# Kernel optimization log

Hardware: AMD Instinct MI355X
Metric: run time of the kernel (lower is better)

## Reference

```python
import jax, jax.numpy as jnp
import numpy as np

N_NODES = 100000
N_EDGES = 3200000
IN_DIM, HID, OUT_DIM = 1, 64, 1


def graph_conv(x, src, dst, ew, W_rel, b_rel, W_root):
    # PyG GraphConv (aggr='add'): out_i = W_rel @ sum_{j->i} w_ij x_j + b_rel + W_root @ x_i
    msg = x[src] * ew[:, None]                               # [E, F]
    agg = jax.ops.segment_sum(msg, dst, num_segments=N_NODES)  # [N, F]
    return agg @ W_rel + b_rel + x @ W_root


def setup_inputs() -> dict:
    key = jax.random.key(0)
    ks = jax.random.split(key, 12)
    def glorot(k, shape):
        fan_in, fan_out = shape
        lim = float(np.sqrt(6.0 / (fan_in + fan_out)))
        return jax.random.uniform(k, shape, jnp.float32, -lim, lim)
    x = jax.random.normal(ks[0], (N_NODES, IN_DIM), jnp.float32)
    edge_index = jax.random.randint(ks[1], (2, N_EDGES), 0, N_NODES, jnp.int64)
    edge_weight = jax.random.uniform(ks[2], (N_EDGES,), jnp.float32)
    return {
        "x": x, "edge_index": edge_index, "edge_weight": edge_weight,
        "W1_rel": glorot(ks[3], (IN_DIM, HID)), "b1": jnp.zeros((HID,), jnp.float32),
        "W1_root": glorot(ks[4], (IN_DIM, HID)),
        "W2_rel": glorot(ks[5], (HID, HID)), "b2": jnp.zeros((HID,), jnp.float32),
        "W2_root": glorot(ks[6], (HID, HID)),
        "W3_rel": glorot(ks[7], (HID, OUT_DIM)), "b3": jnp.zeros((OUT_DIM,), jnp.float32),
        "W3_root": glorot(ks[8], (HID, OUT_DIM)),
    }


def reference(x, edge_index, edge_weight, W1_rel, b1, W1_root, W2_rel, b2, W2_root, W3_rel, b3, W3_root):
    src, dst = edge_index[0], edge_index[1]
    h = graph_conv(x, src, dst, edge_weight, W1_rel, b1, W1_root)
    h = jax.nn.relu(h)  # dropout is identity in eval mode
    h = graph_conv(h, src, dst, edge_weight, W2_rel, b2, W2_root)
    h = jax.nn.relu(h)
    return graph_conv(h, src, dst, edge_weight, W3_rel, b3, W3_root)
```

## Files before the change

### kernel.cpp

```cpp
#include <hip/hip_runtime.h>

#define NN 100000
#define NE 3200000
#define HID 64
#define NPB 256
#define NB  ((NN + NPB - 1) / NPB)
#define NNP (NB * NPB)
#define CAP 9216
#define MNP 128
#define NMW (2 * NB)
#define CAPW 5120
#define CHUNK 4096
#define NCH ((NE + CHUNK - 1) / CHUNK)
#define AP 72
#define BPITCH 136
#define SRCM 0x1FFFF

typedef _Float16 half8 __attribute__((ext_vector_type(8)));
typedef _Float16 h2v   __attribute__((ext_vector_type(2)));
typedef float f32x4 __attribute__((ext_vector_type(4)));

__device__ __forceinline__ unsigned short f2hb(float v) {
    _Float16 h = (_Float16)v;
    unsigned short s;
    __builtin_memcpy(&s, &h, 2);
    return s;
}
__device__ __forceinline__ h2v ash2(unsigned int u) {
    h2v r;
    __builtin_memcpy(&r, &u, 4);
    return r;
}

__global__ __launch_bounds__(512) void k_init(const float* __restrict__ x,
                                              float2* __restrict__ sx,
                                              int* __restrict__ gcur) {
    const int i = blockIdx.x * 512 + threadIdx.x;
    if (i < NN) sx[i] = make_float2(0.f, x[i]);
    if (blockIdx.x == 0 && threadIdx.x < NB) gcur[threadIdx.x] = threadIdx.x * CAP;
}

__global__ __launch_bounds__(256) void k_scatter(const int* __restrict__ src,
                                                 const int* __restrict__ dst,
                                                 const float* __restrict__ ew,
                                                 int* __restrict__ gcur,
                                                 int2* __restrict__ rec,
                                                 unsigned char* __restrict__ dlb) {
    __shared__ int2 lrec[CHUNK];
    __shared__ unsigned short lb[CHUNK];
    __shared__ unsigned short sidx[CHUNK];
    __shared__ int cnt[NB];
    __shared__ int bme[NB];
    __shared__ int wt8[8];
    const int tid = threadIdx.x;
    const int lane = tid & 63, wvx = tid >> 6;
    for (int j = tid; j < NB; j += 256) cnt[j] = 0;
    __syncthreads();
    const long long b0 = (long long)blockIdx.x * CHUNK;
    const int valid = (int)min((long long)CHUNK, (long long)NE - b0);
    #pragma unroll
    for (int k = 0; k < CHUNK / 256; ++k) {
        int idx = k * 256 + tid;
        if (idx < valid) {
            long long e = b0 + idx;
            int d = dst[e];
            int b = d >> 8;
            lrec[idx] = make_int2(src[e] | ((d & 255) << 17), __float_as_int(ew[e]));
            lb[idx] = (unsigned short)b;
            atomicAdd(&cnt[b], 1);
        }
    }
    __syncthreads();
    int v0 = (tid < NB) ? cnt[tid] : 0;
    int v1 = (tid + 256 < NB) ? cnt[tid + 256] : 0;
    int i0 = v0, i1 = v1;
    #pragma unroll
    for (int off = 1; off < 64; off <<= 1) {
        int t0 = __shfl_up(i0, off, 64);
        int t1 = __shfl_up(i1, off, 64);
        if (lane >= off) { i0 += t0; i1 += t1; }
    }
    if (lane == 63) { wt8[wvx] = i0; wt8[4 + wvx] = i1; }
    __syncthreads();
    int off0 = 0, off1 = 0;
    #pragma unroll
    for (int j = 0; j < 8; ++j) {
        int wt = wt8[j];
        if (j < wvx) off0 += wt;
        if (j < 4 + wvx) off1 += wt;
    }
    const int excl0 = off0 + i0 - v0;
    const int excl1 = off1 + i1 - v1;
    if (tid < NB) {
        int bb = v0 ? atomicAdd(&gcur[tid], v0) : 0;
        bme[tid] = bb - excl0;
        cnt[tid] = excl0;
    }
    if (tid + 256 < NB) {
        int bb = v1 ? atomicAdd(&gcur[tid + 256], v1) : 0;
        bme[tid + 256] = bb - excl1;
        cnt[tid + 256] = excl1;
    }
    __syncthreads();
    #pragma unroll
    for (int k = 0; k < CHUNK / 256; ++k) {
        int idx = k * 256 + tid;
        if (idx < valid) {
            int sp = atomicAdd(&cnt[lb[idx]], 1);
            sidx[sp] = (unsigned short)idx;
        }
    }
    __syncthreads();
    #pragma unroll
    for (int k = 0; k < CHUNK / 256; ++k) {
        int sp = k * 256 + tid;
        if (sp < valid) {
            int idx = sidx[sp];
            int b = lb[idx];
            int2 rc = lrec[idx];
            int go = bme[b] + sp;
            rec[go] = rc;
            dlb[go] = (unsigned char)((rc.x >> 17) & 255);
        }
    }
}

__global__ __launch_bounds__(512) void k_s1(const int* __restrict__ gcur,
                                            const int2* __restrict__ rec,
                                            const float* __restrict__ x,
                                            float* __restrict__ sxf) {
    __shared__ float loc[NPB];
    if (threadIdx.x < NPB) loc[threadIdx.x] = 0.f;
    __syncthreads();
    const int wid = blockIdx.x;
    const int b = wid >> 1, j = wid & 1;
    const int beg = b * CAP, cnt = gcur[b] - beg;
    const int half = (cnt + 1) >> 1;
    const int s0 = beg + j * half;
    const int s1e = beg + min(cnt, j * half + half);
    for (int t = s0 + threadIdx.x; t < s1e; t += 512) {
        int2 rc = rec[t];
        atomicAdd(&loc[rc.x >> 17], __int_as_float(rc.y) * x[rc.x & SRCM]);
    }
    __syncthreads();
    const int i = b * NPB + threadIdx.x;
    if (threadIdx.x < NPB && i < NN) {
        float v = loc[threadIdx.x];
        if (v != 0.f) atomicAdd(&sxf[2 * i], v);
    }
}

__global__ __launch_bounds__(512) void k_pack(const int* __restrict__ gcur,
                                              const int2* __restrict__ rec,
                                              const unsigned char* __restrict__ dlb,
                                              const float2* __restrict__ sx,
                                              int4* __restrict__ rec2q,
                                              int* __restrict__ noff,
                                              unsigned char* __restrict__ ngrp) {
    __shared__ int4 img4[CAPW / 2];
    __shared__ int hist[128];
    __shared__ int exclp[128];
    __shared__ int cur[128];
    __shared__ int wt2[2];
    unsigned short* imgh = (unsigned short*)img4;
    const int tid = threadIdx.x;
    const int lane = tid & 63, wv = tid >> 6;
    const int wid = blockIdx.x;
    const int b = wid >> 1, h = wid & 1;
    for (int j = tid; j < CAPW / 2; j += 512) img4[j] = (int4){0, 0, 0, 0};
    if (tid < 128) hist[tid] = 0;
    __syncthreads();
    const int beg = b * CAP;
    const int cnt = gcur[b] - beg;
    {
        const uchar4* d4 = (const uchar4*)(dlb + beg);
        const int n4 = cnt >> 2;
        for (int t = tid; t < n4; t += 512) {
            uchar4 q = d4[t];
            if ((q.x >> 7) == h) atomicAdd(&hist[q.x & 127], 1);
            if ((q.y >> 7) == h) atomicAdd(&hist[q.y & 127], 1);
            if ((q.z >> 7) == h) atomicAdd(&hist[q.z & 127], 1);
            if ((q.w >> 7) == h) atomicAdd(&hist[q.w & 127], 1);
        }
        for (int t = (n4 << 2) + tid; t < cnt; t += 512) {
            int dl = dlb[beg + t];
            if ((dl >> 7) == h) atomicAdd(&hist[dl & 127], 1);
        }
    }
    __syncthreads();
    int pc = 0, incl = 0;
    if (tid < 128) { pc = (hist[tid] + 7) & ~7; incl = pc; }
    #pragma unroll
    for (int off = 1; off < 64; off <<= 1) {
        int tt = __shfl_up(incl, off, 64);
        if (lane >= off) incl += tt;
    }
    if (tid < 128 && lane == 63) wt2[wv] = incl;
    __syncthreads();
    if (tid < 128) {
        int e0 = ((tid >= 64) ? wt2[0] : 0) + incl - pc;
        exclp[tid] = e0;
        cur[tid] = e0;
        const int node = wid * MNP + tid;
        noff[node] = wid * CAPW + e0;
        ngrp[node] = (unsigned char)(pc >> 3);
    }
    __syncthreads();
#define PREC(RX, RY) {                                                  \
        const int dl_ = ((RX) >> 17) & 255;                             \
        if ((dl_ >> 7) == h) {                                          \
            const float w_ = __int_as_float(RY);                        \
            const float2 v_ = sx[(RX) & SRCM];                          \
            int gs_ = atomicAdd(&cur[dl_ & 127], 1);                    \
            int hb_ = (gs_ >> 1) * 8 + (gs_ & 1);                       \
            imgh[hb_]     = f2hb(w_ * v_.x);                            \
            imgh[hb_ + 2] = f2hb(w_ * v_.y);                            \
            imgh[hb_ + 4] = f2hb(w_);                                   \
        } }
    {
        const int4* r4 = (const int4*)(rec + beg);
        const int n2 = cnt >> 1;
        for (int t = tid; t < n2; t += 512) {
            int4 q = r4[t];
            PREC(q.x, q.y)
            PREC(q.z, q.w)
        }
        for (int t = (n2 << 1) + tid; t < cnt; t += 512) {
            int2 rc = rec[beg + t];
            PREC(rc.x, rc.y)
        }
    }
#undef PREC
    __syncthreads();
    int4* d4 = rec2q + (size_t)wid * (CAPW / 2);
    for (int j = tid; j < CAPW / 2; j += 512) d4[j] = img4[j];
}

__global__ __launch_bounds__(512) void k_mega(
        const int* __restrict__ noff, const unsigned char* __restrict__ ngrp,
        const char* __restrict__ rec2b, const float2* __restrict__ sx,
        const float* __restrict__ W1_rel, const float* __restrict__ W1_root,
        const float* __restrict__ b1,
        const float* __restrict__ W2_rel, const float* __restrict__ b2,
        const float* __restrict__ W2_root,
        const float* __restrict__ W3_rel, const float* __restrict__ W3_root,
        const float* __restrict__ b3,
        float* __restrict__ p, float* __restrict__ out) {
    __shared__ _Float16 aggh[MNP * AP];
    __shared__ _Float16 Bt[HID * BPITCH];
    __shared__ float2 sxl[MNP];
    const int tid = threadIdx.x;
    const int f = tid & 63;
    const int wv = tid >> 6;
    const int gi0 = blockIdx.x * MNP;

    for (int j = tid; j < MNP * AP / 2; j += 512) ((int*)aggh)[j] = 0;
    for (int idx = tid; idx < HID * HID; idx += 512) {
        int k = idx >> 6, n = idx & 63;
        Bt[n * BPITCH + k]       = (_Float16)W2_rel[idx];
        Bt[n * BPITCH + HID + k] = (_Float16)W2_root[idx];
    }
    if (tid < MNP) {
        int gi = gi0 + tid;
        sxl[tid] = (gi < NN) ? sx[gi] : make_float2(0.f, 0.f);
    }
    const float w1rf = W1_rel[f], w1tf = W1_root[f], b1ff = b1[f];
    const float b3v = b3[0];
    __syncthreads();

    {
        const int first = gi0 + wv * 16;
        int soff = __builtin_amdgcn_readfirstlane(noff[first]);
        const int4 gvv = *(const int4*)(ngrp + first);
        unsigned ua = __builtin_amdgcn_readfirstlane((unsigned)gvv.x);
        unsigned ub = __builtin_amdgcn_readfirstlane((unsigned)gvv.y);
        unsigned uc = __builtin_amdgcn_readfirstlane((unsigned)gvv.z);
        unsigned ud = __builtin_amdgcn_readfirstlane((unsigned)gvv.w);
        unsigned long long clo = (unsigned long long)ua | ((unsigned long long)ub << 32);
        unsigned long long chi = (unsigned long long)uc | ((unsigned long long)ud << 32);
        #define BSUM(u) (((u) & 255u) + (((u) >> 8) & 255u) + (((u) >> 16) & 255u) + ((u) >> 24))
        const int tg = (int)(BSUM(ua) + BSUM(ub) + BSUM(uc) + BSUM(ud));
        #undef BSUM

        const h2v w1r2 = {(_Float16)w1rf, (_Float16)w1rf};
        const h2v w1t2 = {(_Float16)w1tf, (_Float16)w1tf};
        const h2v b1f2 = {(_Float16)b1ff, (_Float16)b1ff};
        const h2v one2 = {(_Float16)1.f, (_Float16)1.f};
        const h2v zero2 = {(_Float16)0.f, (_Float16)0.f};

        float a0 = 0.f, a1 = 0.f, a2 = 0.f, a3 = 0.f;
        int nrow = wv * 16;
        const int rowend = nrow + 16;
        int grem = (int)(clo & 255); clo = (clo >> 8) | (chi << 56); chi >>= 8;
        while (grem == 0 && nrow + 1 < rowend) {
            ++nrow; grem = (int)(clo & 255);
            clo = (clo >> 8) | (chi << 56); chi >>= 8;
        }

        const int4* rp = (const int4*)rec2b + (soff >> 1);
        int4 A0, A1, A2, A3, B0, B1, B2, B3, C0, C1, C2, C3, D0, D1, D2, D3;
        if (tg >= 1) { A0 = rp[0]; A1 = rp[1]; A2 = rp[2];  A3 = rp[3]; }
        if (tg >= 2) { B0 = rp[4]; B1 = rp[5]; B2 = rp[6];  B3 = rp[7]; }
        if (tg >= 3) { C0 = rp[8]; C1 = rp[9]; C2 = rp[10]; C3 = rp[11]; }
        rp += 12;

#define PP(Q, AA) {                                          \
        h2v z_ = ash2((unsigned)(Q).z) * b1f2;               \
        z_ = ash2((unsigned)(Q).y) * w1t2 + z_;              \
        z_ = ash2((unsigned)(Q).x) * w1r2 + z_;              \
        z_ = __builtin_elementwise_max(z_, zero2);           \
        AA = __builtin_amdgcn_fdot2(z_, one2, AA, false); }

#define BNDRY() {                                                        \
        if (--grem == 0) {                                               \
            aggh[nrow * AP + f] = (_Float16)((a0 + a1) + (a2 + a3));     \
            a0 = a1 = a2 = a3 = 0.f;                                     \
            ++nrow; grem = (int)(clo & 255);                             \
            clo = (clo >> 8) | (chi << 56); chi >>= 8;                   \
            while (grem == 0 && nrow + 1 < rowend) {                     \
                ++nrow; grem = (int)(clo & 255);                         \
                clo = (clo >> 8) | (chi << 56); chi >>= 8;               \
            }                                                            \
        } }

        int t = 0;
        while (t + 4 <= tg) {
            D0 = rp[0]; D1 = rp[1]; D2 = rp[2]; D3 = rp[3];
            PP(A0, a0) PP(A1, a1) PP(A2, a2) PP(A3, a3) BNDRY(); ++t;
            A0 = rp[4]; A1 = rp[5]; A2 = rp[6]; A3 = rp[7];
            PP(B0, a0) PP(B1, a1) PP(B2, a2) PP(B3, a3) BNDRY(); ++t;
            B0 = rp[8]; B1 = rp[9]; B2 = rp[10]; B3 = rp[11];
            PP(C0, a0) PP(C1, a1) PP(C2, a2) PP(C3, a3) BNDRY(); ++t;
            C0 = rp[12]; C1 = rp[13]; C2 = rp[14]; C3 = rp[15];
            PP(D0, a0) PP(D1, a1) PP(D2, a2) PP(D3, a3) BNDRY(); ++t;
            rp += 16;
        }
        if (t < tg) {
            PP(A0, a0) PP(A1, a1) PP(A2, a2) PP(A3, a3) BNDRY(); ++t;
            if (t < tg) {
                PP(B0, a0) PP(B1, a1) PP(B2, a2) PP(B3, a3) BNDRY(); ++t;
                if (t < tg) {
                    PP(C0, a0) PP(C1, a1) PP(C2, a2) PP(C3, a3) BNDRY(); ++t;
                }
            }
        }
#undef PP
#undef BNDRY
    }
    __syncthreads();

    const int m16 = tid & 15;
    const int quad = (tid & 63) >> 4;
    f32x4 acc[4];
    #pragma unroll
    for (int c_ = 0; c_ < 4; ++c_) acc[c_] = (f32x4){0.f, 0.f, 0.f, 0.f};

    const float2 sm = sxl[wv * 16 + m16];

    #pragma unroll
    for (int kt = 0; kt < 4; ++kt) {
        const int kk = kt * 32;
        half8 af;
        if (kt < 2) {
            af = *(const half8*)&aggh[(wv * 16 + m16) * AP + kk + quad * 8];
        } else {
            const int fk0 = (kt - 2) * 32 + quad * 8;
            #pragma unroll
            for (int j = 0; j < 8; ++j) {
                const float wr = W1_rel[fk0 + j], wt = W1_root[fk0 + j], bb = b1[fk0 + j];
                af[j] = (_Float16)fmaxf(0.f, fmaf(sm.x, wr, fmaf(sm.y, wt, bb)));
            }
        }
        #pragma unroll
        for (int ct = 0; ct < 4; ++ct) {
            const half8 bfrag = *(const half8*)&Bt[(ct * 16 + m16) * BPITCH + kk + quad * 8];
            acc[ct] = __builtin_amdgcn_mfma_f32_16x16x32_f16(af, bfrag, acc[ct], 0, 0, 0);
        }
    }

    float b2c[4], w3rc[4], w3tc[4];
    #pragma unroll
    for (int ct = 0; ct < 4; ++ct) {
        const int col = ct * 16 + m16;
        b2c[ct] = b2[col]; w3rc[ct] = W3_rel[col]; w3tc[ct] = W3_root[col];
    }
    float pv[4] = {0.f, 0.f, 0.f, 0.f}, rv[4] = {0.f, 0.f, 0.f, 0.f};
    #pragma unroll
    for (int ct = 0; ct < 4; ++ct) {
        #pragma unroll
        for (int reg = 0; reg < 4; ++reg) {
            const float h2_ = fmaxf(0.f, acc[ct][reg] + b2c[ct]);
            pv[reg] = fmaf(h2_, w3rc[ct], pv[reg]);
            rv[reg] = fmaf(h2_, w3tc[ct], rv[reg]);
        }
    }
    #pragma unroll
    for (int reg = 0; reg < 4; ++reg) {
        #pragma unroll
        for (int msk = 1; msk < 16; msk <<= 1) {
            pv[reg] += __shfl_xor(pv[reg], msk, 64);
            rv[reg] += __shfl_xor(rv[reg], msk, 64);
        }
    }
    if (m16 == 0) {
        #pragma unroll
        for (int reg = 0; reg < 4; ++reg) {
            const int gi = gi0 + wv * 16 + quad * 4 + reg;
            if (gi < NN) { p[gi] = pv[reg]; out[gi] = rv[reg] + b3v; }
        }
    }
}

__global__ __launch_bounds__(512) void k_out(const int* __restrict__ gcur,
                                             const int2* __restrict__ rec,
                                             const float* __restrict__ pp,
                                             float* __restrict__ out) {
    __shared__ float loc[NPB];
    if (threadIdx.x < NPB) loc[threadIdx.x] = 0.f;
    __syncthreads();
    const int wid = blockIdx.x;
    const int b = wid >> 1, j = wid & 1;
    const int beg = b * CAP, cnt = gcur[b] - beg;
    const int half = (cnt + 1) >> 1;
    const int s0 = beg + j * half;
    const int s1e = beg + min(cnt, j * half + half);
    for (int t = s0 + threadIdx.x; t < s1e; t += 512) {
        int2 rc = rec[t];
        atomicAdd(&loc[rc.x >> 17], __int_as_float(rc.y) * pp[rc.x & SRCM]);
    }
    __syncthreads();
    const int i = b * NPB + threadIdx.x;
    if (threadIdx.x < NPB && i < NN) {
        float v = loc[threadIdx.x];
        if (v != 0.f) atomicAdd(&out[i], v);
    }
}

extern "C" void kernel_launch(void* const* d_in, const int* in_sizes, int n_in,
                              void* d_out, int out_size, void* d_ws, size_t ws_size,
                              hipStream_t stream) {
    const float* x       = (const float*)d_in[0];
    const int*   ei      = (const int*)  d_in[1];
    const float* ew      = (const float*)d_in[2];
    const float* W1_rel  = (const float*)d_in[3];
    const float* b1      = (const float*)d_in[4];
    const float* W1_root = (const float*)d_in[5];
    const float* W2_rel  = (const float*)d_in[6];
    const float* b2      = (const float*)d_in[7];
    const float* W2_root = (const float*)d_in[8];
    const float* W3_rel  = (const float*)d_in[9];
    const float* b3      = (const float*)d_in[10];
    const float* W3_root = (const float*)d_in[11];

    const int* src = ei;
    const int* dst = ei + NE;

    const size_t REC_SLOTS = (size_t)NB * CAP;
    int2*          rec   = (int2*)d_ws;
    float2*        sx    = (float2*)(rec + REC_SLOTS);
    float*         p     = (float*)(sx + NN);
    int*           noff  = (int*)(p + NN);
    unsigned char* ngrp  = (unsigned char*)(noff + NNP);
    int*           gcur  = (int*)(ngrp + NNP);
    unsigned char* dlb   = (unsigned char*)(gcur + NB);
    char*          tail  = (char*)(dlb + REC_SLOTS);
    size_t         off   = ((size_t)(tail - (char*)d_ws) + 15) & ~(size_t)15;
    char*          rec2  = (char*)d_ws + off;

    k_init<<<(NN + 511) / 512, 512, 0, stream>>>(x, sx, gcur);
    k_scatter<<<NCH, 256, 0, stream>>>(src, dst, ew, gcur, rec, dlb);
    k_s1<<<2 * NB, 512, 0, stream>>>(gcur, rec, x, (float*)sx);
    k_pack<<<NMW, 512, 0, stream>>>(gcur, rec, dlb, sx, (int4*)rec2, noff, ngrp);
    k_mega<<<NMW, 512, 0, stream>>>(noff, ngrp, rec2, sx,
                                    W1_rel, W1_root, b1,
                                    W2_rel, b2, W2_root,
                                    W3_rel, W3_root, b3, p, (float*)d_out);
    k_out<<<2 * NB, 512, 0, stream>>>(gcur, rec, p, (float*)d_out);
}
```

Baseline: 252.6 us.

## Split edge records into SoA planes with fp16 edge weights

Edge records move from interleaved int2 (packed index plus fp32 weight) to separate planes: a 32-bit packed src/dst-local array and a 16-bit fp16 weight array. The separate dst-local byte array is dropped because that value is now read back from the packed index. The packed fp16 stream used by the mega kernel is also split into three 16-bit planes (w*agg, w*x, w). This cuts the bytes written and read across scatter, s1, pack and out, and gives the mega kernel simpler contiguous loads. In exchange, edge weights are rounded to fp16 in the first-layer and output aggregations, which costs accuracy, and the mega kernel now issues three streams of loads instead of one.

Result: faster. 247.6 us (-2.0%).

```diff
diff --git a/kernel.cpp b/kernel.cpp
--- a/kernel.cpp
+++ b/kernel.cpp
@@ -26,6 +26,12 @@
     __builtin_memcpy(&s, &h, 2);
     return s;
 }
+__device__ __forceinline__ float h2f(unsigned int u) {
+    unsigned short s = (unsigned short)u;
+    _Float16 h;
+    __builtin_memcpy(&h, &s, 2);
+    return (float)h;
+}
 __device__ __forceinline__ h2v ash2(unsigned int u) {
     h2v r;
     __builtin_memcpy(&r, &u, 4);
@@ -44,9 +50,10 @@
                                                  const int* __restrict__ dst,
                                                  const float* __restrict__ ew,
                                                  int* __restrict__ gcur,
-                                                 int2* __restrict__ rec,
-                                                 unsigned char* __restrict__ dlb) {
-    __shared__ int2 lrec[CHUNK];
+                                                 int* __restrict__ rec_a,
+                                                 unsigned short* __restrict__ rec_w) {
+    __shared__ int la[CHUNK];
+    __shared__ unsigned short lw[CHUNK];
     __shared__ unsigned short lb[CHUNK];
     __shared__ unsigned short sidx[CHUNK];
     __shared__ int cnt[NB];
@@ -65,7 +72,8 @@
             long long e = b0 + idx;
             int d = dst[e];
             int b = d >> 8;
-            lrec[idx] = make_int2(src[e] | ((d & 255) << 17), __float_as_int(ew[e]));
+            la[idx] = src[e] | ((d & 255) << 17);
+            lw[idx] = f2hb(ew[e]);
             lb[idx] = (unsigned short)b;
             atomicAdd(&cnt[b], 1);
         }
@@ -117,16 +125,16 @@
         if (sp < valid) {
             int idx = sidx[sp];
             int b = lb[idx];
-            int2 rc = lrec[idx];
             int go = bme[b] + sp;
-            rec[go] = rc;
-            dlb[go] = (unsigned char)((rc.x >> 17) & 255);
+            rec_a[go] = la[idx];
+            rec_w[go] = lw[idx];
         }
     }
 }
 
 __global__ __launch_bounds__(512) void k_s1(const int* __restrict__ gcur,
-                                            const int2* __restrict__ rec,
+                                            const int* __restrict__ rec_a,
+                                            const unsigned short* __restrict__ rec_w,
                                             const float* __restrict__ x,
                                             float* __restrict__ sxf) {
     __shared__ float loc[NPB];
@@ -139,8 +147,9 @@
     const int s0 = beg + j * half;
     const int s1e = beg + min(cnt, j * half + half);
     for (int t = s0 + threadIdx.x; t < s1e; t += 512) {
-        int2 rc = rec[t];
-        atomicAdd(&loc[rc.x >> 17], __int_as_float(rc.y) * x[rc.x & SRCM]);
+        const int a = rec_a[t];
+        const float w = h2f(rec_w[t]);
+        atomicAdd(&loc[a >> 17], w * x[a & SRCM]);
     }
     __syncthreads();
     const int i = b * NPB + threadIdx.x;
@@ -151,39 +160,45 @@
 }
 
 __global__ __launch_bounds__(512) void k_pack(const int* __restrict__ gcur,
-                                              const int2* __restrict__ rec,
-                                              const unsigned char* __restrict__ dlb,
+                                              const int* __restrict__ rec_a,
+                                              const unsigned short* __restrict__ rec_w,
                                               const float2* __restrict__ sx,
-                                              int4* __restrict__ rec2q,
+                                              unsigned short* __restrict__ rec2s,
+                                              unsigned short* __restrict__ rec2x,
+                                              unsigned short* __restrict__ rec2f,
                                               int* __restrict__ noff,
                                               unsigned char* __restrict__ ngrp) {
-    __shared__ int4 img4[CAPW / 2];
+    __shared__ int4 imgq[3 * CAPW / 8];
     __shared__ int hist[128];
     __shared__ int exclp[128];
     __shared__ int cur[128];
     __shared__ int wt2[2];
-    unsigned short* imgh = (unsigned short*)img4;
+    unsigned short* img = (unsigned short*)imgq;
+    unsigned short* ws_img = img;
+    unsigned short* wx_img = img + CAPW;
+    unsigned short* wf_img = img + 2 * CAPW;
     const int tid = threadIdx.x;
     const int lane = tid & 63, wv = tid >> 6;
     const int wid = blockIdx.x;
     const int b = wid >> 1, h = wid & 1;
-    for (int j = tid; j < CAPW / 2; j += 512) img4[j] = (int4){0, 0, 0, 0};
+    for (int j = tid; j < 3 * CAPW / 8; j += 512) imgq[j] = (int4){0, 0, 0, 0};
     if (tid < 128) hist[tid] = 0;
     __syncthreads();
     const int beg = b * CAP;
     const int cnt = gcur[b] - beg;
     {
-        const uchar4* d4 = (const uchar4*)(dlb + beg);
+        const int4* a4 = (const int4*)(rec_a + beg);
         const int n4 = cnt >> 2;
         for (int t = tid; t < n4; t += 512) {
-            uchar4 q = d4[t];
-            if ((q.x >> 7) == h) atomicAdd(&hist[q.x & 127], 1);
-            if ((q.y >> 7) == h) atomicAdd(&hist[q.y & 127], 1);
-            if ((q.z >> 7) == h) atomicAdd(&hist[q.z & 127], 1);
-            if ((q.w >> 7) == h) atomicAdd(&hist[q.w & 127], 1);
+            int4 q = a4[t];
+            int d0 = q.x >> 17, d1 = q.y >> 17, d2 = q.z >> 17, d3 = q.w >> 17;
+            if ((d0 >> 7) == h) atomicAdd(&hist[d0 & 127], 1);
+            if ((d1 >> 7) == h) atomicAdd(&hist[d1 & 127], 1);
+            if ((d2 >> 7) == h) atomicAdd(&hist[d2 & 127], 1);
+            if ((d3 >> 7) == h) atomicAdd(&hist[d3 & 127], 1);
         }
         for (int t = (n4 << 2) + tid; t < cnt; t += 512) {
-            int dl = dlb[beg + t];
+            int dl = rec_a[beg + t] >> 17;
             if ((dl >> 7) == h) atomicAdd(&hist[dl & 127], 1);
         }
     }
@@ -206,39 +221,51 @@
         ngrp[node] = (unsigned char)(pc >> 3);
     }
     __syncthreads();
-#define PREC(RX, RY) {                                                  \
-        const int dl_ = ((RX) >> 17) & 255;                             \
+#define PREC(AA, WW) {                                                  \
+        const int dl_ = (AA) >> 17;                                     \
         if ((dl_ >> 7) == h) {                                          \
-            const float w_ = __int_as_float(RY);                        \
-            const float2 v_ = sx[(RX) & SRCM];                          \
+            const float w_ = h2f(WW);                                   \
+            const float2 v_ = sx[(AA) & SRCM];                          \
             int gs_ = atomicAdd(&cur[dl_ & 127], 1);                    \
-            int hb_ = (gs_ >> 1) * 8 + (gs_ & 1);                       \
-            imgh[hb_]     = f2hb(w_ * v_.x);                            \
-            imgh[hb_ + 2] = f2hb(w_ * v_.y);                            \
-            imgh[hb_ + 4] = f2hb(w_);                                   \
+            ws_img[gs_] = f2hb(w_ * v_.x);                              \
+            wx_img[gs_] = f2hb(w_ * v_.y);                              \
+            wf_img[gs_] = (unsigned short)(WW);                         \
         } }
     {
-        const int4* r4 = (const int4*)(rec + beg);
-        const int n2 = cnt >> 1;
-        for (int t = tid; t < n2; t += 512) {
-            int4 q = r4[t];
-            PREC(q.x, q.y)
-            PREC(q.z, q.w)
-        }
-        for (int t = (n2 << 1) + tid; t < cnt; t += 512) {
-            int2 rc = rec[beg + t];
-            PREC(rc.x, rc.y)
+        const int4* a4 = (const int4*)(rec_a + beg);
+        const ushort4* w4 = (const ushort4*)(rec_w + beg);
+        const int n4 = cnt >> 2;
+        for (int t = tid; t < n4; t += 512) {
+            int4 qa = a4[t];
+            ushort4 qw = w4[t];
+            PREC(qa.x, qw.x)
+            PREC(qa.y, qw.y)
+            PREC(qa.z, qw.z)
+            PREC(qa.w, qw.w)
+        }
+        for (int t = (n4 << 2) + tid; t < cnt; t += 512) {
+            PREC(rec_a[beg + t], rec_w[beg + t])
         }
     }
 #undef PREC
     __syncthreads();
-    int4* d4 = rec2q + (size_t)wid * (CAPW / 2);
-    for (int j = tid; j < CAPW / 2; j += 512) d4[j] = img4[j];
+    {
+        const size_t pb = (size_t)wid * (CAPW / 8);
+        int4* d0 = (int4*)rec2s + pb;
+        int4* d1 = (int4*)rec2x + pb;
+        int4* d2 = (int4*)rec2f + pb;
+        for (int j = tid; j < CAPW / 8; j += 512) d0[j] = imgq[j];
+        for (int j = tid; j < CAPW / 8; j += 512) d1[j] = imgq[CAPW / 8 + j];
+        for (int j = tid; j < CAPW / 8; j += 512) d2[j] = imgq[2 * (CAPW / 8) + j];
+    }
 }
 
 __global__ __launch_bounds__(512) void k_mega(
         const int* __restrict__ noff, const unsigned char* __restrict__ ngrp,
-        const char* __restrict__ rec2b, const float2* __restrict__ sx,
+        const unsigned short* __restrict__ rec2s,
+        const unsigned short* __restrict__ rec2x,
+        const unsigned short* __restrict__ rec2f,
+        const float2* __restrict__ sx,
         const float* __restrict__ W1_rel, const float* __restrict__ W1_root,
         const float* __restrict__ b1,
         const float* __restrict__ W2_rel, const float* __restrict__ b2,
@@ -297,19 +324,25 @@
             clo = (clo >> 8) | (chi << 56); chi >>= 8;
         }
 
-        const int4* rp = (const int4*)rec2b + (soff >> 1);
-        int4 A0, A1, A2, A3, B0, B1, B2, B3, C0, C1, C2, C3, D0, D1, D2, D3;
-        if (tg >= 1) { A0 = rp[0]; A1 = rp[1]; A2 = rp[2];  A3 = rp[3]; }
-        if (tg >= 2) { B0 = rp[4]; B1 = rp[5]; B2 = rp[6];  B3 = rp[7]; }
-        if (tg >= 3) { C0 = rp[8]; C1 = rp[9]; C2 = rp[10]; C3 = rp[11]; }
-        rp += 12;
-
-#define PP(Q, AA) {                                          \
-        h2v z_ = ash2((unsigned)(Q).z) * b1f2;               \
-        z_ = ash2((unsigned)(Q).y) * w1t2 + z_;              \
-        z_ = ash2((unsigned)(Q).x) * w1r2 + z_;              \
+        const int4* ps = (const int4*)rec2s + (soff >> 3);
+        const int4* px = (const int4*)rec2x + (soff >> 3);
+        const int4* pf = (const int4*)rec2f + (soff >> 3);
+
+        int4 S0, X0, F0, S1, X1, F1, S2, X2, F2, S3, X3, F3;
+        if (tg >= 1) { S0 = ps[0]; X0 = px[0]; F0 = pf[0]; }
+        if (tg >= 2) { S1 = ps[1]; X1 = px[1]; F1 = pf[1]; }
+        if (tg >= 3) { S2 = ps[2]; X2 = px[2]; F2 = pf[2]; }
+
+#define PP(SS, XX, FF, AA) {                                 \
+        h2v z_ = ash2((unsigned)(FF)) * b1f2;                \
+        z_ = ash2((unsigned)(XX)) * w1t2 + z_;               \
+        z_ = ash2((unsigned)(SS)) * w1r2 + z_;               \
         z_ = __builtin_elementwise_max(z_, zero2);           \
         AA = __builtin_amdgcn_fdot2(z_, one2, AA, false); }
+
+#define GRP(S, X, F)                                         \
+        PP(S.x, X.x, F.x, a0) PP(S.y, X.y, F.y, a1)          \
+        PP(S.z, X.z, F.z, a2) PP(S.w, X.w, F.w, a3)
 
 #define BNDRY() {                                                        \
         if (--grem == 0) {                                               \
@@ -325,26 +358,26 @@
 
         int t = 0;
         while (t + 4 <= tg) {
-            D0 = rp[0]; D1 = rp[1]; D2 = rp[2]; D3 = rp[3];
-            PP(A0, a0) PP(A1, a1) PP(A2, a2) PP(A3, a3) BNDRY(); ++t;
-            A0 = rp[4]; A1 = rp[5]; A2 = rp[6]; A3 = rp[7];
-            PP(B0, a0) PP(B1, a1) PP(B2, a2) PP(B3, a3) BNDRY(); ++t;
-            B0 = rp[8]; B1 = rp[9]; B2 = rp[10]; B3 = rp[11];
-            PP(C0, a0) PP(C1, a1) PP(C2, a2) PP(C3, a3) BNDRY(); ++t;
-            C0 = rp[12]; C1 = rp[13]; C2 = rp[14]; C3 = rp[15];
-            PP(D0, a0) PP(D1, a1) PP(D2, a2) PP(D3, a3) BNDRY(); ++t;
-            rp += 16;
+            S3 = ps[t + 3]; X3 = px[t + 3]; F3 = pf[t + 3];
+            GRP(S0, X0, F0) BNDRY(); ++t;
+            S0 = ps[t + 3]; X0 = px[t + 3]; F0 = pf[t + 3];
+            GRP(S1, X1, F1) BNDRY(); ++t;
+            S1 = ps[t + 3]; X1 = px[t + 3]; F1 = pf[t + 3];
+            GRP(S2, X2, F2) BNDRY(); ++t;
+            S2 = ps[t + 3]; X2 = px[t + 3]; F2 = pf[t + 3];
+            GRP(S3, X3, F3) BNDRY(); ++t;
         }
         if (t < tg) {
-            PP(A0, a0) PP(A1, a1) PP(A2, a2) PP(A3, a3) BNDRY(); ++t;
+            GRP(S0, X0, F0) BNDRY(); ++t;
             if (t < tg) {
-                PP(B0, a0) PP(B1, a1) PP(B2, a2) PP(B3, a3) BNDRY(); ++t;
+                GRP(S1, X1, F1) BNDRY(); ++t;
                 if (t < tg) {
-                    PP(C0, a0) PP(C1, a1) PP(C2, a2) PP(C3, a3) BNDRY(); ++t;
+                    GRP(S2, X2, F2) BNDRY(); ++t;
                 }
             }
         }
 #undef PP
+#undef GRP
 #undef BNDRY
     }
     __syncthreads();
@@ -412,7 +445,8 @@
 }
 
 __global__ __launch_bounds__(512) void k_out(const int* __restrict__ gcur,
-                                             const int2* __restrict__ rec,
+                                             const int* __restrict__ rec_a,
+                                             const unsigned short* __restrict__ rec_w,
                                              const float* __restrict__ pp,
                                              float* __restrict__ out) {
     __shared__ float loc[NPB];
@@ -425,8 +459,9 @@
     const int s0 = beg + j * half;
     const int s1e = beg + min(cnt, j * half + half);
     for (int t = s0 + threadIdx.x; t < s1e; t += 512) {
-        int2 rc = rec[t];
-        atomicAdd(&loc[rc.x >> 17], __int_as_float(rc.y) * pp[rc.x & SRCM]);
+        const int a = rec_a[t];
+        const float w = h2f(rec_w[t]);
+        atomicAdd(&loc[a >> 17], w * pp[a & SRCM]);
     }
     __syncthreads();
     const int i = b * NPB + threadIdx.x;
@@ -456,24 +491,28 @@
     const int* dst = ei + NE;
 
     const size_t REC_SLOTS = (size_t)NB * CAP;
-    int2*          rec   = (int2*)d_ws;
-    float2*        sx    = (float2*)(rec + REC_SLOTS);
-    float*         p     = (float*)(sx + NN);
-    int*           noff  = (int*)(p + NN);
-    unsigned char* ngrp  = (unsigned char*)(noff + NNP);
-    int*           gcur  = (int*)(ngrp + NNP);
-    unsigned char* dlb   = (unsigned char*)(gcur + NB);
-    char*          tail  = (char*)(dlb + REC_SLOTS);
-    size_t         off   = ((size_t)(tail - (char*)d_ws) + 15) & ~(size_t)15;
-    char*          rec2  = (char*)d_ws + off;
+    const size_t PLANE     = (size_t)NMW * CAPW;
+    int*            rec_a = (int*)d_ws;
+    unsigned short* rec_w = (unsigned short*)(rec_a + REC_SLOTS);
+    float2*         sx    = (float2*)(rec_w + REC_SLOTS);
+    float*          p     = (float*)(sx + NN);
+    int*            noff  = (int*)(p + NN);
+    unsigned char*  ngrp  = (unsigned char*)(noff + NNP);
+    int*            gcur  = (int*)(ngrp + NNP);
+    char*           tail  = (char*)(gcur + NB);
+    size_t          off   = ((size_t)(tail - (char*)d_ws) + 15) & ~(size_t)15;
+    unsigned short* rec2s = (unsigned short*)((char*)d_ws + off);
+    unsigned short* rec2x = rec2s + PLANE;
+    unsigned short* rec2f = rec2x + PLANE;
 
     k_init<<<(NN + 511) / 512, 512, 0, stream>>>(x, sx, gcur);
-    k_scatter<<<NCH, 256, 0, stream>>>(src, dst, ew, gcur, rec, dlb);
-    k_s1<<<2 * NB, 512, 0, stream>>>(gcur, rec, x, (float*)sx);
-    k_pack<<<NMW, 512, 0, stream>>>(gcur, rec, dlb, sx, (int4*)rec2, noff, ngrp);
-    k_mega<<<NMW, 512, 0, stream>>>(noff, ngrp, rec2, sx,
+    k_scatter<<<NCH, 256, 0, stream>>>(src, dst, ew, gcur, rec_a, rec_w);
+    k_s1<<<2 * NB, 512, 0, stream>>>(gcur, rec_a, rec_w, x, (float*)sx);
+    k_pack<<<NMW, 512, 0, stream>>>(gcur, rec_a, rec_w, sx,
+                                    rec2s, rec2x, rec2f, noff, ngrp);
+    k_mega<<<NMW, 512, 0, stream>>>(noff, ngrp, rec2s, rec2x, rec2f, sx,
                                     W1_rel, W1_root, b1,
                                     W2_rel, b2, W2_root,
                                     W3_rel, W3_root, b3, p, (float*)d_out);
-    k_out<<<2 * NB, 512, 0, stream>>>(gcur, rec, p, (float*)d_out);
-}
+    k_out<<<2 * NB, 512, 0, stream>>>(gcur, rec_a, rec_w, p, (float*)d_out);
+}
```
